# Optimization experiments

Measured on AMD Instinct MI355X. Metric: run time of the kernel, lower is better.

Reference implementation:

```python
import jax, jax.numpy as jnp
import numpy as np
import math

B, S, H, DM, DFF = 8, 512, 16, 1024, 4096
DK = DM // H
EPS = 1e-6


def setup_inputs() -> dict:
    key = jax.random.key(0)
    ks = jax.random.split(key, 12)
    rn = lambda k, shape, s=0.02: (jax.random.normal(k, shape, jnp.float32) * s)
    return dict(
        x=jax.random.normal(ks[0], (B, S, DM), jnp.float32),
        mask=jnp.ones((B, 1, 1, S), jnp.int32),
        Wq=rn(ks[1], (DM, DM)), bq=jnp.zeros((DM,), jnp.float32),
        Wk=rn(ks[2], (DM, DM)), bk=jnp.zeros((DM,), jnp.float32),
        Wv=rn(ks[3], (DM, DM)), bv=jnp.zeros((DM,), jnp.float32),
        Wo=rn(ks[4], (DM, DM)), bo=jnp.zeros((DM,), jnp.float32),
        r_k=rn(ks[5], (S, S, DK)),
        r_v=rn(ks[6], (S, S, DK)),
        ln1_g=jnp.ones((DM,), jnp.float32), ln1_b=jnp.zeros((DM,), jnp.float32),
        ln2_g=jnp.ones((DM,), jnp.float32), ln2_b=jnp.zeros((DM,), jnp.float32),
        w1=rn(ks[7], (DFF, DM)), b1=jnp.zeros((DFF,), jnp.float32),
        w2=rn(ks[8], (DM, DFF)), b2=jnp.zeros((DM,), jnp.float32),
    )


def _layernorm(x, g, b):
    # torch: std with Bessel correction (ddof=1), divide by (std + eps)
    mean = jnp.mean(x, axis=-1, keepdims=True)
    std = jnp.std(x, axis=-1, keepdims=True, ddof=1)
    return g * (x - mean) / (std + EPS) + b


def _gelu_tanh(x):
    c = math.sqrt(2.0 / math.pi)
    return 0.5 * x * (1.0 + jnp.tanh(c * (x + 0.044715 * x * x * x)))


def _attention(xn, mask, Wq, bq, Wk, bk, Wv, bv, Wo, bo, r_k, r_v):
    def heads(x, W, bias):
        y = x @ W.T + bias                      # [B,S,DM]
        return y.reshape(B, S, H, DK).transpose(0, 2, 1, 3)  # [B,H,S,DK]
    q, k, v = heads(xn, Wq, bq), heads(xn, Wk, bk), heads(xn, Wv, bv)
    scale = 1.0 / math.sqrt(DK)
    scores = jnp.einsum('bhqd,bhkd->bhqk', q, k) * scale
    rel_score = jnp.einsum('bhqd,qkd->bhqk', q, r_k)  # relative-position bias
    scores = scores + rel_score * scale
    scores = jnp.where(mask == 0, -1e9, scores)
    p = jax.nn.softmax(scores, axis=-1)
    out = jnp.einsum('bhqk,bhkd->bhqd', p, v) + jnp.einsum('bhqk,qkd->bhqd', p, r_v)
    out = out.transpose(0, 2, 1, 3).reshape(B, S, DM)
    return out @ Wo.T + bo


def reference(x, mask, Wq, bq, Wk, bk, Wv, bv, Wo, bo, r_k, r_v,
              ln1_g, ln1_b, ln2_g, ln2_b, w1, b1, w2, b2):
    # sublayer 1: x + attn(LN(x))
    x = x + _attention(_layernorm(x, ln1_g, ln1_b), mask,
                       Wq, bq, Wk, bk, Wv, bv, Wo, bo, r_k, r_v)
    # sublayer 2: x + FFN(LN(x))
    h = _layernorm(x, ln2_g, ln2_b)
    h = _gelu_tanh(h @ w1.T + b1) @ w2.T + b2
    return x + h
```

## Files before the change

kernel.cpp:

```cpp
#include <hip/hip_runtime.h>
#include <math.h>


typedef unsigned short ushort_t;
typedef __attribute__((ext_vector_type(8))) short short8;
typedef __attribute__((ext_vector_type(4))) float f32x4;
typedef __attribute__((ext_vector_type(8))) __bf16 bf16x8;

__device__ __forceinline__ float b2f(ushort_t u) {
  unsigned v = (unsigned)u << 16;
  return __builtin_bit_cast(float, v);
}
__device__ __forceinline__ ushort_t f2b(float f) {
  unsigned x = __builtin_bit_cast(unsigned, f);
  x = x + 0x7fffu + ((x >> 16) & 1u);
  return (ushort_t)(x >> 16);
}

__device__ __forceinline__ void gload16(const ushort_t* g, ushort_t* l) {
  __builtin_amdgcn_global_load_lds(
      (const __attribute__((address_space(1))) unsigned*)g,
      (__attribute__((address_space(3))) unsigned*)l, 16, 0, 0);
}

__global__ void k_f32_to_bf16(const float* __restrict__ in,
                              ushort_t* __restrict__ out, long long n) {
  long long i = ((long long)blockIdx.x * blockDim.x + threadIdx.x) * 4;
  if (i >= n) return;
  float4 v = *reinterpret_cast<const float4*>(in + i);
  ushort4 o;
  o.x = f2b(v.x); o.y = f2b(v.y); o.z = f2b(v.z); o.w = f2b(v.w);
  *reinterpret_cast<ushort4*>(out + i) = o;
}

__global__ void k_layernorm_bf16(const float* __restrict__ x,
                                 const float* __restrict__ g,
                                 const float* __restrict__ b,
                                 ushort_t* __restrict__ out) {
  const int lane = threadIdx.x & 63;
  const int row = (blockIdx.x << 2) + (threadIdx.x >> 6);
  const float* xr = x + (long long)row * 1024;
  float4 v[4];
  float s = 0.f, ss = 0.f;
#pragma unroll
  for (int i = 0; i < 4; ++i) {
    v[i] = *reinterpret_cast<const float4*>(xr + lane * 16 + i * 4);
    s += v[i].x + v[i].y + v[i].z + v[i].w;
    ss += v[i].x * v[i].x + v[i].y * v[i].y + v[i].z * v[i].z + v[i].w * v[i].w;
  }
#pragma unroll
  for (int o = 32; o > 0; o >>= 1) {
    s += __shfl_xor(s, o);
    ss += __shfl_xor(ss, o);
  }
  float mean = s * (1.f / 1024.f);
  float var = (ss - 1024.f * mean * mean) * (1.f / 1023.f);
  var = fmaxf(var, 0.f);
  float inv = 1.f / (sqrtf(var) + 1e-6f);
  ushort_t* orow = out + (long long)row * 1024;
#pragma unroll
  for (int i = 0; i < 4; ++i) {
    int c = lane * 16 + i * 4;
    ushort4 o;
    o.x = f2b(g[c + 0] * (v[i].x - mean) * inv + b[c + 0]);
    o.y = f2b(g[c + 1] * (v[i].y - mean) * inv + b[c + 1]);
    o.z = f2b(g[c + 2] * (v[i].z - mean) * inv + b[c + 2]);
    o.w = f2b(g[c + 3] * (v[i].w - mean) * inv + b[c + 3]);
    *reinterpret_cast<ushort4*>(orow + c) = o;
  }
}

__global__ void k_softmax(ushort_t* __restrict__ sc, const int* __restrict__ mask,
                          float scale) {
  const int lane = threadIdx.x & 63;
  const long long row = ((long long)blockIdx.x << 2) + (threadIdx.x >> 6);
  const int b = (int)(row >> 13);
  ushort_t* srow = sc + row * 512;
  const int* mrow = mask + b * 512;
  short8 sv = *reinterpret_cast<const short8*>(srow + lane * 8);
  float vals[8];
  float mx = -1e30f;
#pragma unroll
  for (int j = 0; j < 8; ++j) {
    float f = b2f((ushort_t)sv[j]) * scale;
    if (mrow[lane * 8 + j] == 0) f = -1e9f;
    vals[j] = f;
    mx = fmaxf(mx, f);
  }
#pragma unroll
  for (int o = 32; o > 0; o >>= 1) mx = fmaxf(mx, __shfl_xor(mx, o));
  float s = 0.f;
#pragma unroll
  for (int j = 0; j < 8; ++j) {
    vals[j] = __expf(vals[j] - mx);
    s += vals[j];
  }
#pragma unroll
  for (int o = 32; o > 0; o >>= 1) s += __shfl_xor(s, o);
  float inv = 1.f / s;
  short8 ov;
#pragma unroll
  for (int j = 0; j < 8; ++j) ov[j] = (short)f2b(vals[j] * inv);
  *reinterpret_cast<short8*>(srow + lane * 8) = ov;
}

__global__ void k_transpose_v(const ushort_t* __restrict__ v,
                              ushort_t* __restrict__ vT) {
  __shared__ ushort_t tls[64][72];
  const int bh = blockIdx.y;
  const int s0 = blockIdx.x << 6;
  const int t = threadIdx.x;
  const long long base = (long long)bh * 32768;
#pragma unroll
  for (int it = 0; it < 2; ++it) {
    int r = (t >> 3) + it * 32;
    int c = (t & 7) << 3;
    short8 val = *reinterpret_cast<const short8*>(v + base + (long long)(s0 + r) * 64 + c);
    *reinterpret_cast<short8*>(&tls[r][c]) = val;
  }
  __syncthreads();
#pragma unroll
  for (int it = 0; it < 2; ++it) {
    int d = (t >> 3) + it * 32;
    int cs = (t & 7) << 3;
    short8 o;
#pragma unroll
    for (int j = 0; j < 8; ++j) o[j] = (short)tls[cs + j][d];
    *reinterpret_cast<short8*>(vT + base + (long long)d * 512 + s0 + cs) = o;
  }
}

__global__ void k_transpose_rv(const float* __restrict__ rv,
                               ushort_t* __restrict__ rvT) {
  __shared__ float tls[64][65];
  const int q = blockIdx.y;
  const int k0 = blockIdx.x << 6;
  const int t = threadIdx.x;
  const long long ibase = (long long)q * 32768;
#pragma unroll
  for (int it = 0; it < 4; ++it) {
    int r = (t >> 4) + it * 16;
    int c = (t & 15) << 2;
    float4 val = *reinterpret_cast<const float4*>(rv + ibase + (long long)(k0 + r) * 64 + c);
    tls[r][c] = val.x; tls[r][c + 1] = val.y; tls[r][c + 2] = val.z; tls[r][c + 3] = val.w;
  }
  __syncthreads();
#pragma unroll
  for (int it = 0; it < 2; ++it) {
    int d = (t >> 3) + it * 32;
    int cs = (t & 7) << 3;
    short8 o;
#pragma unroll
    for (int j = 0; j < 8; ++j) o[j] = (short)f2b(tls[cs + j][d]);
    *reinterpret_cast<short8*>(rvT + ibase + (long long)d * 512 + k0 + cs) = o;
  }
}

__global__ void k_reshape_attn(const ushort_t* __restrict__ a,
                               ushort_t* __restrict__ o) {
  long long i = (long long)blockIdx.x * 256 + threadIdx.x;
  int col8 = (int)(i & 127);
  long long tok = i >> 7;
  int col = col8 << 3;
  int h = col >> 6, d = col & 63;
  int bb = (int)(tok >> 9), s = (int)(tok & 511);
  short8 v = *reinterpret_cast<const short8*>(
      a + ((long long)(bb * 16 + h) * 512 + s) * 64 + d);
  *reinterpret_cast<short8*>(o + (tok << 10) + col) = v;
}

struct GArgs {
  const ushort_t* A; const ushort_t* B;
  long long a_bs, b_bs, c_bs;
  long long a_rs, b_rs, c_rs;
  int M, N, K;
  float scale;
  ushort_t* Cb;
  float* Cf;
  const float* bias;
  const float* resid;
  ushort_t* qb; ushort_t* kb; ushort_t* vb;
};

template <int MODE>
__global__ __launch_bounds__(256) void k_gemm_bt(GArgs g) {
  __shared__ ushort_t As[128 * 32];
  __shared__ ushort_t Bs[128 * 32];
  const int t = threadIdx.x;
  const int lane = t & 63;
  const int w = t >> 6, wr = w >> 1, wc = w & 1;
  const long long z = blockIdx.z;
  const int m0 = blockIdx.y * 128, n0 = blockIdx.x * 128;
  const ushort_t* Ab = g.A + z * g.a_bs;
  const ushort_t* Bb = g.B + z * g.b_bs;
  const int sr = t >> 2;
  const int sc = (t & 3) << 3;
  const long long ar0 = min(m0 + sr, g.M - 1);
  const long long ar1 = min(m0 + sr + 64, g.M - 1);
  const long long br0 = min(n0 + sr, g.N - 1);
  const long long br1 = min(n0 + sr + 64, g.N - 1);
  const ushort_t* Ap0 = Ab + ar0 * g.a_rs + sc;
  const ushort_t* Ap1 = Ab + ar1 * g.a_rs + sc;
  const ushort_t* Bp0 = Bb + br0 * g.b_rs + sc;
  const ushort_t* Bp1 = Bb + br1 * g.b_rs + sc;
  ushort_t* AsW0 = As + w * 512;
  ushort_t* AsW1 = As + 2048 + w * 512;
  ushort_t* BsW0 = Bs + w * 512;
  ushort_t* BsW1 = Bs + 2048 + w * 512;

  f32x4 acc[4][4];
#pragma unroll
  for (int i = 0; i < 4; ++i)
#pragma unroll
    for (int j = 0; j < 4; ++j) acc[i][j] = f32x4{0.f, 0.f, 0.f, 0.f};

  const int fr = lane & 15;
  const int fkb = (lane >> 4) << 3;
  const int a_off0 = (wr * 64 + fr) * 32 + fkb;
  const int b_off0 = (wc * 64 + fr) * 32 + fkb;

  const int nkt = g.K >> 5;
  for (int kt = 0; kt < nkt; ++kt) {
    const int k0 = kt << 5;
    __syncthreads();
    gload16(Ap0 + k0, AsW0);
    gload16(Ap1 + k0, AsW1);
    gload16(Bp0 + k0, BsW0);
    gload16(Bp1 + k0, BsW1);
    __syncthreads();
    bf16x8 af[4], bfv[4];
#pragma unroll
    for (int i = 0; i < 4; ++i)
      af[i] = *reinterpret_cast<const bf16x8*>(&As[a_off0 + i * 16 * 32]);
#pragma unroll
    for (int j = 0; j < 4; ++j)
      bfv[j] = *reinterpret_cast<const bf16x8*>(&Bs[b_off0 + j * 16 * 32]);
#pragma unroll
    for (int i = 0; i < 4; ++i)
#pragma unroll
      for (int j = 0; j < 4; ++j)
        acc[i][j] = __builtin_amdgcn_mfma_f32_16x16x32_bf16(af[i], bfv[j],
                                                            acc[i][j], 0, 0, 0);
  }

  const int er0 = wr * 64 + ((lane >> 4) << 2);
  const int ec0 = wc * 64 + (lane & 15);
#pragma unroll
  for (int i = 0; i < 4; ++i) {
#pragma unroll
    for (int j = 0; j < 4; ++j) {
#pragma unroll
      for (int r = 0; r < 4; ++r) {
        int row = m0 + er0 + i * 16 + r;
        int col = n0 + ec0 + j * 16;
        if (row >= g.M || col >= g.N) continue;
        float val = acc[i][j][r] * g.scale;
        if constexpr (MODE == 0) {
          g.Cb[z * g.c_bs + (long long)row * g.c_rs + col] = f2b(val);
        } else if constexpr (MODE == 1) {
          long long idx = z * g.c_bs + (long long)row * g.c_rs + col;
          g.Cb[idx] = f2b(b2f(g.Cb[idx]) + val);
        } else if constexpr (MODE == 2) {
          val += g.bias[col];
          int which = col >> 10;
          int h = (col >> 6) & 15;
          int d = col & 63;
          int bb = row >> 9, s = row & 511;
          ushort_t* dst = (which == 0) ? g.qb : (which == 1) ? g.kb : g.vb;
          dst[((long long)(bb * 16 + h) * 512 + s) * 64 + d] = f2b(val);
        } else if constexpr (MODE == 3) {
          long long idx = z * g.c_bs + (long long)row * g.c_rs + col;
          g.Cf[idx] = g.resid[idx] + val + g.bias[col];
        } else if constexpr (MODE == 4) {
          float xv = val + g.bias[col];
          float tv = tanhf(0.7978845608028654f * (xv + 0.044715f * xv * xv * xv));
          g.Cb[z * g.c_bs + (long long)row * g.c_rs + col] =
              f2b(0.5f * xv * (1.f + tv));
        }
      }
    }
  }
}

extern "C" void kernel_launch(void* const* d_in, const int* in_sizes, int n_in,
                              void* d_out, int out_size, void* d_ws,
                              size_t ws_size, hipStream_t stream) {
  const float* x    = (const float*)d_in[0];
  const int*   mask = (const int*)d_in[1];
  const float* Wq   = (const float*)d_in[2];
  const float* bq   = (const float*)d_in[3];
  const float* Wk   = (const float*)d_in[4];
  const float* bk   = (const float*)d_in[5];
  const float* Wv   = (const float*)d_in[6];
  const float* bv   = (const float*)d_in[7];
  const float* Wo   = (const float*)d_in[8];
  const float* bo   = (const float*)d_in[9];
  const float* r_k  = (const float*)d_in[10];
  const float* r_v  = (const float*)d_in[11];
  const float* ln1g = (const float*)d_in[12];
  const float* ln1b = (const float*)d_in[13];
  const float* ln2g = (const float*)d_in[14];
  const float* ln2b = (const float*)d_in[15];
  const float* w1   = (const float*)d_in[16];
  const float* b1   = (const float*)d_in[17];
  const float* w2   = (const float*)d_in[18];
  const float* b2   = (const float*)d_in[19];
  float* out = (float*)d_out;

  char* ws = (char*)d_ws;
  size_t off = 0;
  auto alloc = [&](size_t bytes) -> void* {
    void* p = ws + off;
    off += (bytes + 255) & ~(size_t)255;
    return p;
  };
  ushort_t* wqkv = (ushort_t*)alloc(3072ll * 1024 * 2);
  ushort_t* wo_b = (ushort_t*)alloc(1024ll * 1024 * 2);
  ushort_t* w1_b = (ushort_t*)alloc(4096ll * 1024 * 2);
  ushort_t* w2_b = (ushort_t*)alloc(1024ll * 4096 * 2);
  ushort_t* rk_b = (ushort_t*)alloc(512ll * 512 * 64 * 2);
  ushort_t* rvT  = (ushort_t*)alloc(512ll * 64 * 512 * 2);
  ushort_t* xn   = (ushort_t*)alloc(4096ll * 1024 * 2);
  ushort_t* qb   = (ushort_t*)alloc(128ll * 512 * 64 * 2);
  ushort_t* kb   = (ushort_t*)alloc(128ll * 512 * 64 * 2);
  ushort_t* vb   = (ushort_t*)alloc(128ll * 512 * 64 * 2);
  ushort_t* vT   = (ushort_t*)alloc(128ll * 64 * 512 * 2);
  ushort_t* scp  = (ushort_t*)alloc(128ll * 512 * 512 * 2);
  ushort_t* attn = (ushort_t*)alloc(128ll * 512 * 64 * 2);
  float*    x1   = (float*)alloc(4096ll * 1024 * 4);
  float*    bqkv = (float*)alloc(3072 * 4);
  ushort_t* attn_tok = xn;
  ushort_t* h_b = qb;
  ushort_t* mid = scp;

  hipMemcpyAsync(bqkv, bq, 1024 * 4, hipMemcpyDeviceToDevice, stream);
  hipMemcpyAsync(bqkv + 1024, bk, 1024 * 4, hipMemcpyDeviceToDevice, stream);
  hipMemcpyAsync(bqkv + 2048, bv, 1024 * 4, hipMemcpyDeviceToDevice, stream);

  auto cvt = [&](const float* src, ushort_t* dst, long long n) {
    k_f32_to_bf16<<<dim3((unsigned)((n / 4 + 255) / 256)), 256, 0, stream>>>(src, dst, n);
  };
  cvt(Wq, wqkv, 1024ll * 1024);
  cvt(Wk, wqkv + 1024ll * 1024, 1024ll * 1024);
  cvt(Wv, wqkv + 2048ll * 1024, 1024ll * 1024);
  cvt(Wo, wo_b, 1024ll * 1024);
  cvt(w1, w1_b, 4096ll * 1024);
  cvt(w2, w2_b, 1024ll * 4096);
  cvt(r_k, rk_b, 512ll * 512 * 64);
  k_transpose_rv<<<dim3(8, 512), 256, 0, stream>>>(r_v, rvT);

  k_layernorm_bf16<<<1024, 256, 0, stream>>>(x, ln1g, ln1b, xn);

  {
    GArgs a{};
    a.A = xn; a.B = wqkv; a.a_rs = 1024; a.b_rs = 1024;
    a.M = 4096; a.N = 3072; a.K = 1024; a.scale = 1.f;
    a.bias = bqkv; a.qb = qb; a.kb = kb; a.vb = vb;
    k_gemm_bt<2><<<dim3(24, 32, 1), 256, 0, stream>>>(a);
  }

  k_transpose_v<<<dim3(8, 128), 256, 0, stream>>>(vb, vT);

  {
    GArgs s{};
    s.A = qb; s.B = kb; s.a_bs = 32768; s.b_bs = 32768; s.c_bs = 262144;
    s.a_rs = 64; s.b_rs = 64; s.c_rs = 512;
    s.M = 512; s.N = 512; s.K = 64; s.scale = 1.f; s.Cb = scp;
    k_gemm_bt<0><<<dim3(4, 4, 128), 256, 0, stream>>>(s);
  }
  {
    GArgs r{};
    r.A = qb; r.B = rk_b; r.a_bs = 64; r.b_bs = 32768; r.c_bs = 512;
    r.a_rs = 32768; r.b_rs = 64; r.c_rs = 262144;
    r.M = 128; r.N = 512; r.K = 64; r.scale = 1.f; r.Cb = scp;
    k_gemm_bt<1><<<dim3(4, 1, 512), 256, 0, stream>>>(r);
  }

  k_softmax<<<16384, 256, 0, stream>>>(scp, mask, 0.125f);

  {
    GArgs pv{};
    pv.A = scp; pv.B = vT; pv.a_bs = 262144; pv.b_bs = 32768; pv.c_bs = 32768;
    pv.a_rs = 512; pv.b_rs = 512; pv.c_rs = 64;
    pv.M = 512; pv.N = 64; pv.K = 512; pv.scale = 1.f; pv.Cb = attn;
    k_gemm_bt<0><<<dim3(1, 4, 128), 256, 0, stream>>>(pv);
  }
  {
    GArgs pr{};
    pr.A = scp; pr.B = rvT; pr.a_bs = 512; pr.b_bs = 32768; pr.c_bs = 64;
    pr.a_rs = 262144; pr.b_rs = 512; pr.c_rs = 32768;
    pr.M = 128; pr.N = 64; pr.K = 512; pr.scale = 1.f; pr.Cb = attn;
    k_gemm_bt<1><<<dim3(1, 1, 512), 256, 0, stream>>>(pr);
  }

  k_reshape_attn<<<2048, 256, 0, stream>>>(attn, attn_tok);

  {
    GArgs o{};
    o.A = attn_tok; o.B = wo_b; o.a_rs = 1024; o.b_rs = 1024; o.c_rs = 1024;
    o.M = 4096; o.N = 1024; o.K = 1024; o.scale = 1.f;
    o.Cf = x1; o.bias = bo; o.resid = x;
    k_gemm_bt<3><<<dim3(8, 32, 1), 256, 0, stream>>>(o);
  }

  k_layernorm_bf16<<<1024, 256, 0, stream>>>(x1, ln2g, ln2b, h_b);

  {
    GArgs f1{};
    f1.A = h_b; f1.B = w1_b; f1.a_rs = 1024; f1.b_rs = 1024; f1.c_rs = 4096;
    f1.M = 4096; f1.N = 4096; f1.K = 1024; f1.scale = 1.f;
    f1.Cb = mid; f1.bias = b1;
    k_gemm_bt<4><<<dim3(32, 32, 1), 256, 0, stream>>>(f1);
  }
  {
    GArgs f2{};
    f2.A = mid; f2.B = w2_b; f2.a_rs = 4096; f2.b_rs = 4096; f2.c_rs = 1024;
    f2.M = 4096; f2.N = 1024; f2.K = 4096; f2.scale = 1.f;
    f2.Cf = out; f2.bias = b2; f2.resid = x1;
    k_gemm_bt<3><<<dim3(8, 32, 1), 256, 0, stream>>>(f2);
  }
}
```

Before: 637.6 us.

## Double-buffer GEMM LDS tiles and swizzle block order across XCDs

Reworks the bf16 MFMA GEMM to use two LDS buffers, so the async global-to-LDS loads for the next K tile are issued while the current tile is being consumed. This drops one barrier per iteration and overlaps load latency with MFMA work. It also adds an optional block-index remap that spreads neighbouring tiles across the chip's 8 XCDs, meant to improve L2 reuse of A/B panels. The remap is enabled for the QKV, output-projection and FFN GEMMs. The cost is doubled LDS usage per block, which may lower occupancy.

```diff
diff --git a/kernel.cpp b/kernel.cpp
--- a/kernel.cpp
+++ b/kernel.cpp
@@ -180,17 +180,29 @@
   const float* bias;
   const float* resid;
   ushort_t* qb; ushort_t* kb; ushort_t* vb;
+  int swz;
 };
 
 template <int MODE>
 __global__ __launch_bounds__(256) void k_gemm_bt(GArgs g) {
-  __shared__ ushort_t As[128 * 32];
-  __shared__ ushort_t Bs[128 * 32];
+  __shared__ ushort_t As[2][128 * 32];
+  __shared__ ushort_t Bs[2][128 * 32];
   const int t = threadIdx.x;
   const int lane = t & 63;
   const int w = t >> 6, wr = w >> 1, wc = w & 1;
   const long long z = blockIdx.z;
-  const int m0 = blockIdx.y * 128, n0 = blockIdx.x * 128;
+
+  int bx = blockIdx.x, by = blockIdx.y;
+  if (g.swz) {
+    int nx = gridDim.x;
+    int id = by * nx + bx;
+    int cpx = (nx * gridDim.y) >> 3;
+    id = (id & 7) * cpx + (id >> 3);
+    bx = id % nx;
+    by = id / nx;
+  }
+  const int m0 = by * 128, n0 = bx * 128;
+
   const ushort_t* Ab = g.A + z * g.a_bs;
   const ushort_t* Bb = g.B + z * g.b_bs;
   const int sr = t >> 2;
@@ -203,10 +215,7 @@
   const ushort_t* Ap1 = Ab + ar1 * g.a_rs + sc;
   const ushort_t* Bp0 = Bb + br0 * g.b_rs + sc;
   const ushort_t* Bp1 = Bb + br1 * g.b_rs + sc;
-  ushort_t* AsW0 = As + w * 512;
-  ushort_t* AsW1 = As + 2048 + w * 512;
-  ushort_t* BsW0 = Bs + w * 512;
-  ushort_t* BsW1 = Bs + 2048 + w * 512;
+  const int wofs = w * 512;
 
   f32x4 acc[4][4];
 #pragma unroll
@@ -220,21 +229,29 @@
   const int b_off0 = (wc * 64 + fr) * 32 + fkb;
 
   const int nkt = g.K >> 5;
+  gload16(Ap0, &As[0][wofs]);
+  gload16(Ap1, &As[0][2048 + wofs]);
+  gload16(Bp0, &Bs[0][wofs]);
+  gload16(Bp1, &Bs[0][2048 + wofs]);
+
   for (int kt = 0; kt < nkt; ++kt) {
-    const int k0 = kt << 5;
+    const int cur = kt & 1;
     __syncthreads();
-    gload16(Ap0 + k0, AsW0);
-    gload16(Ap1 + k0, AsW1);
-    gload16(Bp0 + k0, BsW0);
-    gload16(Bp1 + k0, BsW1);
-    __syncthreads();
+    if (kt + 1 < nkt) {
+      const int k0 = (kt + 1) << 5;
+      const int nxt = cur ^ 1;
+      gload16(Ap0 + k0, &As[nxt][wofs]);
+      gload16(Ap1 + k0, &As[nxt][2048 + wofs]);
+      gload16(Bp0 + k0, &Bs[nxt][wofs]);
+      gload16(Bp1 + k0, &Bs[nxt][2048 + wofs]);
+    }
     bf16x8 af[4], bfv[4];
 #pragma unroll
     for (int i = 0; i < 4; ++i)
-      af[i] = *reinterpret_cast<const bf16x8*>(&As[a_off0 + i * 16 * 32]);
+      af[i] = *reinterpret_cast<const bf16x8*>(&As[cur][a_off0 + i * 512]);
 #pragma unroll
     for (int j = 0; j < 4; ++j)
-      bfv[j] = *reinterpret_cast<const bf16x8*>(&Bs[b_off0 + j * 16 * 32]);
+      bfv[j] = *reinterpret_cast<const bf16x8*>(&Bs[cur][b_off0 + j * 512]);
 #pragma unroll
     for (int i = 0; i < 4; ++i)
 #pragma unroll
@@ -355,7 +372,7 @@
     GArgs a{};
     a.A = xn; a.B = wqkv; a.a_rs = 1024; a.b_rs = 1024;
     a.M = 4096; a.N = 3072; a.K = 1024; a.scale = 1.f;
-    a.bias = bqkv; a.qb = qb; a.kb = kb; a.vb = vb;
+    a.bias = bqkv; a.qb = qb; a.kb = kb; a.vb = vb; a.swz = 1;
     k_gemm_bt<2><<<dim3(24, 32, 1), 256, 0, stream>>>(a);
   }
 
@@ -399,7 +416,7 @@
     GArgs o{};
     o.A = attn_tok; o.B = wo_b; o.a_rs = 1024; o.b_rs = 1024; o.c_rs = 1024;
     o.M = 4096; o.N = 1024; o.K = 1024; o.scale = 1.f;
-    o.Cf = x1; o.bias = bo; o.resid = x;
+    o.Cf = x1; o.bias = bo; o.resid = x; o.swz = 1;
     k_gemm_bt<3><<<dim3(8, 32, 1), 256, 0, stream>>>(o);
   }
 
@@ -409,14 +426,14 @@
     GArgs f1{};
     f1.A = h_b; f1.B = w1_b; f1.a_rs = 1024; f1.b_rs = 1024; f1.c_rs = 4096;
     f1.M = 4096; f1.N = 4096; f1.K = 1024; f1.scale = 1.f;
-    f1.Cb = mid; f1.bias = b1;
+    f1.Cb = mid; f1.bias = b1; f1.swz = 1;
     k_gemm_bt<4><<<dim3(32, 32, 1), 256, 0, stream>>>(f1);
   }
   {
     GArgs f2{};
     f2.A = mid; f2.B = w2_b; f2.a_rs = 4096; f2.b_rs = 4096; f2.c_rs = 1024;
     f2.M = 4096; f2.N = 1024; f2.K = 4096; f2.scale = 1.f;
-    f2.Cf = out; f2.bias = b2; f2.resid = x1;
+    f2.Cf = out; f2.bias = b2; f2.resid = x1; f2.swz = 1;
     k_gemm_bt<3><<<dim3(8, 32, 1), 256, 0, stream>>>(f2);
   }
 }
```

Result: faster. 600.5 us (-5.8%).

## Double GEMM K-tile to 64 and XOR-swizzle LDS layout

Applied to the files above, without the earlier changes.

The bf16 MFMA GEMM now stages a 64-wide K slice per iteration instead of 32, which halves the number of barrier pairs and loop iterations per K. It also applies an XOR swizzle on 16-byte chunks in the LDS tiles to avoid bank conflicts on the fragment reads. LDS use per block doubles to 32KB, which could lower occupancy. K must now be a multiple of 64.

```diff
diff --git a/kernel.cpp b/kernel.cpp
--- a/kernel.cpp
+++ b/kernel.cpp
@@ -184,29 +184,28 @@
 
 template <int MODE>
 __global__ __launch_bounds__(256) void k_gemm_bt(GArgs g) {
-  __shared__ ushort_t As[128 * 32];
-  __shared__ ushort_t Bs[128 * 32];
+  __shared__ ushort_t As[128 * 64];
+  __shared__ ushort_t Bs[128 * 64];
   const int t = threadIdx.x;
   const int lane = t & 63;
   const int w = t >> 6, wr = w >> 1, wc = w & 1;
   const long long z = blockIdx.z;
   const int m0 = blockIdx.y * 128, n0 = blockIdx.x * 128;
+
   const ushort_t* Ab = g.A + z * g.a_bs;
   const ushort_t* Bb = g.B + z * g.b_bs;
-  const int sr = t >> 2;
-  const int sc = (t & 3) << 3;
-  const long long ar0 = min(m0 + sr, g.M - 1);
-  const long long ar1 = min(m0 + sr + 64, g.M - 1);
-  const long long br0 = min(n0 + sr, g.N - 1);
-  const long long br1 = min(n0 + sr + 64, g.N - 1);
-  const ushort_t* Ap0 = Ab + ar0 * g.a_rs + sc;
-  const ushort_t* Ap1 = Ab + ar1 * g.a_rs + sc;
-  const ushort_t* Bp0 = Bb + br0 * g.b_rs + sc;
-  const ushort_t* Bp1 = Bb + br1 * g.b_rs + sc;
-  ushort_t* AsW0 = As + w * 512;
-  ushort_t* AsW1 = As + 2048 + w * 512;
-  ushort_t* BsW0 = Bs + w * 512;
-  ushort_t* BsW1 = Bs + 2048 + w * 512;
+
+  const int srow = t >> 3;
+  const int scol = (((t & 7) ^ (srow & 7)) << 3);
+  const ushort_t* Ap[4];
+  const ushort_t* Bp[4];
+#pragma unroll
+  for (int p = 0; p < 4; ++p) {
+    long long ar = min((long long)(m0 + p * 32 + srow), (long long)g.M - 1);
+    long long br = min((long long)(n0 + p * 32 + srow), (long long)g.N - 1);
+    Ap[p] = Ab + ar * g.a_rs + scol;
+    Bp[p] = Bb + br * g.b_rs + scol;
+  }
 
   f32x4 acc[4][4];
 #pragma unroll
@@ -215,36 +214,46 @@
     for (int j = 0; j < 4; ++j) acc[i][j] = f32x4{0.f, 0.f, 0.f, 0.f};
 
   const int fr = lane & 15;
-  const int fkb = (lane >> 4) << 3;
-  const int a_off0 = (wr * 64 + fr) * 32 + fkb;
-  const int b_off0 = (wc * 64 + fr) * 32 + fkb;
-
-  const int nkt = g.K >> 5;
+  const int g4 = lane >> 4;
+  const int fsw = fr & 7;
+
+  const int nkt = g.K >> 6;
   for (int kt = 0; kt < nkt; ++kt) {
-    const int k0 = kt << 5;
+    const int k0 = kt << 6;
     __syncthreads();
-    gload16(Ap0 + k0, AsW0);
-    gload16(Ap1 + k0, AsW1);
-    gload16(Bp0 + k0, BsW0);
-    gload16(Bp1 + k0, BsW1);
+#pragma unroll
+    for (int p = 0; p < 4; ++p) {
+      gload16(Ap[p] + k0, &As[p * 2048 + w * 512]);
+      gload16(Bp[p] + k0, &Bs[p * 2048 + w * 512]);
+    }
     __syncthreads();
-    bf16x8 af[4], bfv[4];
-#pragma unroll
-    for (int i = 0; i < 4; ++i)
-      af[i] = *reinterpret_cast<const bf16x8*>(&As[a_off0 + i * 16 * 32]);
+
+    bf16x8 bfv[4][2];
 #pragma unroll
     for (int j = 0; j < 4; ++j)
-      bfv[j] = *reinterpret_cast<const bf16x8*>(&Bs[b_off0 + j * 16 * 32]);
-#pragma unroll
-    for (int i = 0; i < 4; ++i)
-#pragma unroll
-      for (int j = 0; j < 4; ++j)
-        acc[i][j] = __builtin_amdgcn_mfma_f32_16x16x32_bf16(af[i], bfv[j],
+#pragma unroll
+      for (int kk = 0; kk < 2; ++kk)
+        bfv[j][kk] = *reinterpret_cast<const bf16x8*>(
+            &Bs[(wc * 64 + j * 16 + fr) * 64 + (((kk * 4 + g4) ^ fsw) << 3)]);
+#pragma unroll
+    for (int i = 0; i < 4; ++i) {
+      const int arow = (wr * 64 + i * 16 + fr) * 64;
+      bf16x8 af0 = *reinterpret_cast<const bf16x8*>(
+          &As[arow + ((g4 ^ fsw) << 3)]);
+      bf16x8 af1 = *reinterpret_cast<const bf16x8*>(
+          &As[arow + (((4 + g4) ^ fsw) << 3)]);
+#pragma unroll
+      for (int j = 0; j < 4; ++j) {
+        acc[i][j] = __builtin_amdgcn_mfma_f32_16x16x32_bf16(af0, bfv[j][0],
                                                             acc[i][j], 0, 0, 0);
-  }
-
-  const int er0 = wr * 64 + ((lane >> 4) << 2);
-  const int ec0 = wc * 64 + (lane & 15);
+        acc[i][j] = __builtin_amdgcn_mfma_f32_16x16x32_bf16(af1, bfv[j][1],
+                                                            acc[i][j], 0, 0, 0);
+      }
+    }
+  }
+
+  const int er0 = wr * 64 + (g4 << 2);
+  const int ec0 = wc * 64 + fr;
 #pragma unroll
   for (int i = 0; i < 4; ++i) {
 #pragma unroll
```

Result: no change. 649.4 us (+1.9%).
